# Kernel optimization log

Measured on AMD Instinct MI355X. Metric: run time of the kernel, lower is better.

## Reference

```python
import math
import jax, jax.numpy as jnp
import numpy as np

N_ORDERS = 2
CHUNK = 64  # tokens per chunk (before virtual-token expansion)


def _expand_derivative(x, n):
    """expand_virtual_tokens(mode='derivative'): [B,H,S,D] -> [B,H,S*n,D]."""
    B, H, S, D = x.shape
    pad = jnp.zeros((B, H, n - 1, D), x.dtype)
    xp = jnp.concatenate([pad, x], axis=2)  # [B,H,S+n-1,D]
    coeffs = np.array([(-1) ** kk * math.comb(n - 1, kk) for kk in range(n)], dtype=np.float32)
    coeffs = coeffs / np.abs(coeffs).sum()  # L1-normalized binomial coeffs
    # window j at token t is x_pad[t+j]*coeffs[j]; then flip window dim (as in torch .flip(-1))
    win = jnp.stack([xp[:, :, j:j + S, :] * coeffs[j] for j in range(n)], axis=3)  # [B,H,S,n,D]
    win = win[:, :, :, ::-1, :]
    return win.reshape(B, H, S * n, D)


def _unlinear(x, scale=2.0):
    """unlinear_activation: gated norm-scaled gelu applied to inter-chunk state."""
    xn = jnp.linalg.norm(x, axis=-1, keepdims=True) + 1e-6
    return x / scale * jax.nn.gelu(scale * x / xn, approximate=True)


def _stab(x):
    # ensure_stability: clamp to [-1e4, 1e4], nan -> center (0)
    return jnp.nan_to_num(jnp.clip(x, -1e4, 1e4), nan=0.0, posinf=1e4, neginf=-1e4)


def _forward(q, k, v, beta):
    n = N_ORDERS
    B, H, S, D = q.shape
    qe = _expand_derivative(q, n)
    ke = _expand_derivative(k, n)
    ve = _expand_derivative(v, n)
    be = jnp.repeat(beta, n, axis=-1)[..., None]  # [B,H,S*n,1]
    w = ke * be  # delta-rule write keys
    u = ve * be  # delta-rule write values

    Cn = CHUNK * n                     # virtual tokens per chunk
    NC = (S * n) // Cn                 # number of chunks
    ch = lambda x: x.reshape(B, H, NC, Cn, D)
    qc, kc, wc, uc = ch(qe), ch(ke), ch(w), ch(u)

    # triangular (forward-substitution) inversion per chunk:
    # T = (I + tril(W K^T, -1))^{-1}  == fast_invert_matrix of the strictly-lower system
    A = jnp.tril(jnp.einsum('bhnid,bhnjd->bhnij', wc, kc), -1)
    eye = jnp.eye(Cn, dtype=q.dtype)
    T = jax.scipy.linalg.solve_triangular(
        eye + A, jnp.broadcast_to(eye, A.shape), lower=True, unit_diagonal=True)
    wci = jnp.einsum('bhnij,bhnjd->bhnid', T, wc)
    uci = jnp.einsum('bhnij,bhnjd->bhnid', T, uc)

    def chunk_step(h, xs):
        # sequential_delta_product_scan body: per-token Householder updates, n_orders steps
        qx, wx, ux = xs  # each [B,H,Cn,D]
        C = CHUNK
        qr = qx.reshape(B, H, C, n, D)
        wr = wx.reshape(B, H, C, n, D)
        ur = ux.reshape(B, H, C, n, D)
        state = jnp.broadcast_to(h[:, :, None], (B, H, C, D, D))  # per-token state
        outs = []
        for s in range(n):
            qs, ws, us = qr[:, :, :, s], wr[:, :, :, s], ur[:, :, :, s]
            kho = jnp.einsum('bhcd,bhcde->bhce', ws, state)
            uval = us - kho
            o_inter = jnp.einsum('bhcd,bhcde->bhce', qs, state)
            o_intra = qs * uval
            state = _stab(state + jnp.einsum('bhcd,bhce->bhcde', ws, uval))
            outs.append(o_intra + o_inter)
        o = jnp.stack(outs, axis=3).reshape(B, H, C * n, D)  # interleave: pos t*n+s
        h_new = _unlinear(state[:, :, -1])  # linear_activation=False path
        return h_new, o

    xs = (jnp.moveaxis(qc, 2, 0), jnp.moveaxis(wci, 2, 0), jnp.moveaxis(uci, 2, 0))
    h0 = jnp.zeros((B, H, D, D), q.dtype)
    _, os = jax.lax.scan(chunk_step, h0, xs)  # os: [NC,B,H,Cn,D]
    out_v = jnp.moveaxis(os, 0, 2).reshape(B, H, S, n, D)
    return out_v[..., n - 1, :]  # collapse virtual tokens: keep last-order output per token


def setup_inputs() -> dict:
    key = jax.random.key(0)
    kq, kk, kv, kb = jax.random.split(key, 4)
    B, H, S, D = 2, 16, 2048, 64
    return {
        'q': jax.random.normal(kq, (B, H, S, D), jnp.float32),
        'k': jax.random.normal(kk, (B, H, S, D), jnp.float32),
        'v': jax.random.normal(kv, (B, H, S, D), jnp.float32),
        'beta': jax.random.uniform(kb, (B, H, S), jnp.float32),
    }


def reference(q, k, v, beta):
    return _forward(q, k, v, beta)
```

## Files before the change

kernel.cpp:

```cpp
#include <hip/hip_runtime.h>
#include <math.h>


namespace {
constexpr int PAIRS = 32;
constexpr int SLEN  = 2048;
constexpr int D     = 64;
constexpr int CK    = 64;
constexpr int CN    = 128;
constexpr int NCH   = 32;
constexpr int NB2   = 16;
constexpr int NP    = 5;
constexpr size_t YWORDS = (size_t)PAIRS * NCH * CN * CN;
constexpr int GP = 2145;

__device__ __forceinline__ float stab1(float x) {
    float y = __builtin_amdgcn_fmed3f(x, -10000.f, 10000.f);
    return (x != x) ? 0.f : y;
}

__device__ __forceinline__ int kidx(int a, int f4) {
    return a * 68 + 4 * (f4 ^ ((a >> 2) & 3));
}
}

__global__ __launch_bounds__(256, 2)
void la_gram(const float* __restrict__ kg, float* __restrict__ gG)
{
    __shared__ float kstf[65 * 68];
    const int blk = blockIdx.x;
    const int p = blk >> 5, nc = blk & 31;
    const int tid = threadIdx.x;
    const int baseT = nc * CK;
    const float* kp = kg + (size_t)p * SLEN * D;

    for (int u = tid; u < 65 * 16; u += 256) {
        int a = u >> 4, f4 = u & 15;
        int src = baseT - 1 + a;
        float4 val = float4{0.f, 0.f, 0.f, 0.f};
        if (src >= 0) val = ((const float4*)(kp + (size_t)src * D))[f4];
        *(float4*)&kstf[kidx(a, f4)] = val;
    }
    __syncthreads();

    float* gps = gG + (size_t)blk * GP;
    for (int tt = tid; tt < 17 * 17; tt += 256) {
        int ta = tt / 17, tb = tt % 17;
        if (tb > ta) continue;
        int a0 = ta * 4, b0 = tb * 4;
        float acc[4][4] = {};
        for (int d4 = 0; d4 < 16; ++d4) {
            float4 av[4], bv[4];
            #pragma unroll
            for (int r = 0; r < 4; ++r) {
                av[r] = *(const float4*)&kstf[kidx(min(a0 + r, 64), d4)];
                bv[r] = *(const float4*)&kstf[kidx(min(b0 + r, 64), d4)];
            }
            #pragma unroll
            for (int r = 0; r < 4; ++r)
                #pragma unroll
                for (int c = 0; c < 4; ++c)
                    acc[r][c] += av[r].x * bv[c].x + av[r].y * bv[c].y
                               + av[r].z * bv[c].z + av[r].w * bv[c].w;
        }
        #pragma unroll
        for (int r = 0; r < 4; ++r)
            #pragma unroll
            for (int c = 0; c < 4; ++c) {
                int a = a0 + r, b = b0 + c;
                if (a <= 64 && b <= a)
                    gps[a * (a + 1) / 2 + b] = acc[r][c];
            }
    }
}

__global__ __launch_bounds__(256, 3)
void la_phase1g(const float* __restrict__ kg, const float* __restrict__ vg,
                const float* __restrict__ bg, float* __restrict__ ws,
                const float* __restrict__ gG)
{
    __shared__ float Ysh[CN][64];
    __shared__ float scm[2][CN][8];
    __shared__ float redsh[24][66];
    __shared__ float bq4[CK], bh[CK];

    const int blk  = blockIdx.x;
    const int p    = blk >> 6;
    const int nc   = (blk >> 1) & 31;
    const int half = blk & 1;
    const int tid  = threadIdx.x;
    const int col  = tid & 63;
    const int m    = tid >> 6;
    const int baseT = nc * CK;
    const float* kp = kg + (size_t)p * SLEN * D;
    const float* vp = vg + (size_t)p * SLEN * D;
    const float* bp = bg + (size_t)p * SLEN;
    const float* gps = gG + (size_t)(p * NCH + nc) * GP;

    if (tid < CK) {
        float bv = bp[baseT + tid];
        bq4[tid] = 0.25f * bv;
        bh[tid]  = 0.5f  * bv;
    }
    __syncthreads();

    const float* srcBase = half ? vp : kp;
    for (int u = tid; u < CN * 16; u += 256) {
        int i = u >> 4, f4 = u & 15;
        int ci = i >> 1, si = i & 1;
        float sc = si ? bh[ci] : -bh[ci];
        int srcT = baseT + ci - si;
        float4 val = float4{0.f, 0.f, 0.f, 0.f};
        if (srcT >= 0) val = ((const float4*)(srcBase + (size_t)srcT * D))[f4];
        val.x *= sc; val.y *= sc; val.z *= sc; val.w *= sc;
        *(float4*)&Ysh[i][f4 * 4] = val;
    }
    for (int e = tid; e < 64; e += 256) {
        int j = e >> 3, r = e & 7;
        int ai = (r >> 1) - (r & 1) + 1;
        int aj = (j >> 1) - (j & 1) + 1;
        int amax = max(ai, aj), amin = min(ai, aj);
        float sgn = ((r ^ j) & 1) ? -1.f : 1.f;
        scm[0][j][r] = sgn * bq4[r >> 1] * gps[amax * (amax + 1) / 2 + amin];
    }
    __syncthreads();

    for (int g = 0; g < 16; ++g) {
        const int buf = g & 1;
        float acc[8] = {};
        for (int j = m; j < 8 * g; j += 4) {
            float yv = Ysh[j][col];
            const float4 a03 = *(const float4*)&scm[buf][j][0];
            const float4 a47 = *(const float4*)&scm[buf][j][4];
            acc[0] += a03.x * yv; acc[1] += a03.y * yv;
            acc[2] += a03.z * yv; acc[3] += a03.w * yv;
            acc[4] += a47.x * yv; acc[5] += a47.y * yv;
            acc[6] += a47.z * yv; acc[7] += a47.w * yv;
        }
        if (m > 0) {
            #pragma unroll
            for (int r = 0; r < 8; ++r) redsh[(m - 1) * 8 + r][col] = acc[r];
        }
        __syncthreads();
        if (m == 0) {
            if (g > 0) {
                #pragma unroll
                for (int r = 0; r < 8; ++r)
                    acc[r] += redsh[r][col] + redsh[8 + r][col] + redsh[16 + r][col];
            }
            float yn[8];
            #pragma unroll
            for (int r = 0; r < 8; ++r) {
                float val = Ysh[8 * g + r][col] - acc[r];
                #pragma unroll
                for (int rp = 0; rp < 8; ++rp)
                    if (rp < r) val -= scm[buf][8 * g + rp][r] * yn[rp];
                yn[r] = val;
                Ysh[8 * g + r][col] = val;
            }
        } else if (g < 15) {
            const int T = g + 1, bufB = T & 1;
            const int nel = 8 * (8 * T + 8);
            for (int e = tid - 64; e < nel; e += 192) {
                int j = e >> 3, r = e & 7;
                int i = 8 * T + r;
                int ai = (i >> 1) - (i & 1) + 1;
                int aj = (j >> 1) - (j & 1) + 1;
                int amax = max(ai, aj), amin = min(ai, aj);
                float sgn = ((i ^ j) & 1) ? -1.f : 1.f;
                scm[bufB][j][r] = sgn * bq4[i >> 1] * gps[amax * (amax + 1) / 2 + amin];
            }
        }
        __syncthreads();
    }

    float* gY = ws + (size_t)(p * NCH + nc) * (CN * CN) + half * 64;
    for (int u = tid; u < CN * 16; u += 256) {
        int r = u >> 4, f4 = u & 15;
        *(float4*)&gY[r * CN + f4 * 4] = *(const float4*)&Ysh[r][f4 * 4];
    }
}

__global__ __launch_bounds__(256, 2)
void la_phase1f(const float* __restrict__ kg, const float* __restrict__ vg,
                const float* __restrict__ bg, float* __restrict__ ws)
{
    __shared__ float Ysh[CN][64];
    __shared__ float Gm[65][66];
    __shared__ char  ureg[17680];
    __shared__ float bq4[CK], bh[CK];

    float* kstf = (float*)ureg;
    float* scm  = (float*)ureg;
    float (*redsh)[66] = (float(*)[66])(ureg + 8192);

    const int blk  = blockIdx.x;
    const int p    = blk >> 6;
    const int nc   = (blk >> 1) & 31;
    const int half = blk & 1;
    const int tid  = threadIdx.x;
    const int baseT = nc * CK;
    const float* kp = kg + (size_t)p * SLEN * D;
    const float* vp = vg + (size_t)p * SLEN * D;
    const float* bp = bg + (size_t)p * SLEN;

    for (int u = tid; u < 65 * 16; u += 256) {
        int a = u >> 4, f4 = u & 15;
        int src = baseT - 1 + a;
        float4 val = float4{0.f, 0.f, 0.f, 0.f};
        if (src >= 0) val = ((const float4*)(kp + (size_t)src * D))[f4];
        *(float4*)&kstf[kidx(a, f4)] = val;
    }
    if (tid < CK) {
        float bv = bp[baseT + tid];
        bq4[tid] = 0.25f * bv;
        bh[tid]  = 0.5f  * bv;
    }
    __syncthreads();

    for (int u = tid; u < CN * 16; u += 256) {
        int i = u >> 4, f4 = u & 15;
        int ci = i >> 1, si = i & 1;
        float sc = si ? bh[ci] : -bh[ci];
        float4 val = float4{0.f, 0.f, 0.f, 0.f};
        if (half == 0) {
            val = *(const float4*)&kstf[kidx(ci - si + 1, f4)];
        } else {
            int srcT = baseT + ci - si;
            if (srcT >= 0) val = ((const float4*)(vp + (size_t)srcT * D))[f4];
        }
        val.x *= sc; val.y *= sc; val.z *= sc; val.w *= sc;
        *(float4*)&Ysh[i][f4 * 4] = val;
    }

    for (int tt = tid; tt < 17 * 17; tt += 256) {
        int ta = tt / 17, tb = tt % 17;
        if (tb > ta) continue;
        int a0 = ta * 4, b0 = tb * 4;
        float acc[4][4] = {};
        for (int d4 = 0; d4 < 16; ++d4) {
            float4 av[4], bv[4];
            #pragma unroll
            for (int r = 0; r < 4; ++r) {
                av[r] = *(const float4*)&kstf[kidx(min(a0 + r, 64), d4)];
                bv[r] = *(const float4*)&kstf[kidx(min(b0 + r, 64), d4)];
            }
            #pragma unroll
            for (int r = 0; r < 4; ++r)
                #pragma unroll
                for (int c = 0; c < 4; ++c)
                    acc[r][c] += av[r].x * bv[c].x + av[r].y * bv[c].y
                               + av[r].z * bv[c].z + av[r].w * bv[c].w;
        }
        #pragma unroll
        for (int r = 0; r < 4; ++r)
            #pragma unroll
            for (int c = 0; c < 4; ++c)
                if (a0 + r <= 64 && b0 + c <= 64) {
                    Gm[a0 + r][b0 + c] = acc[r][c];
                    Gm[b0 + c][a0 + r] = acc[r][c];
                }
    }
    __syncthreads();

    auto stripf = [&](int g, int t0, int tstride) {
        int buf = g & 1;
        int jmax = 8 * g + 8;
        for (int e = t0; e < 8 * jmax; e += tstride) {
            int j = e >> 3, r = e & 7;
            int i = 8 * g + r;
            int ai = (i >> 1) - (i & 1) + 1;
            int aj = (j >> 1) - (j & 1) + 1;
            float sgn = ((i ^ j) & 1) ? -1.f : 1.f;
            scm[(buf * CN + j) * 8 + r] = sgn * bq4[i >> 1] * Gm[ai][aj];
        }
    };

    stripf(0, tid, 256);
    __syncthreads();

    const int col = tid & 63;
    const int m   = tid >> 6;
    for (int g = 0; g < 16; ++g) {
        const int buf = g & 1;
        float acc[8] = {};
        for (int j = m; j < 8 * g; j += 4) {
            float yv = Ysh[j][col];
            const float4 a03 = *(const float4*)&scm[(buf * CN + j) * 8];
            const float4 a47 = *(const float4*)&scm[(buf * CN + j) * 8 + 4];
            acc[0] += a03.x * yv; acc[1] += a03.y * yv;
            acc[2] += a03.z * yv; acc[3] += a03.w * yv;
            acc[4] += a47.x * yv; acc[5] += a47.y * yv;
            acc[6] += a47.z * yv; acc[7] += a47.w * yv;
        }
        if (m > 0) {
            #pragma unroll
            for (int r = 0; r < 8; ++r) redsh[(m - 1) * 8 + r][col] = acc[r];
        }
        __syncthreads();
        if (m == 0) {
            if (g > 0) {
                #pragma unroll
                for (int r = 0; r < 8; ++r)
                    acc[r] += redsh[r][col] + redsh[8 + r][col] + redsh[16 + r][col];
            }
            float yn[8];
            #pragma unroll
            for (int r = 0; r < 8; ++r) {
                float val = Ysh[8 * g + r][col] - acc[r];
                #pragma unroll
                for (int rp = 0; rp < 8; ++rp)
                    if (rp < r) val -= scm[(buf * CN + 8 * g + rp) * 8 + r] * yn[rp];
                yn[r] = val;
                Ysh[8 * g + r][col] = val;
            }
        } else if (g < 15) {
            stripf(g + 1, tid - 64, 192);
        }
        __syncthreads();
    }

    float* gY = ws + (size_t)(p * NCH + nc) * (CN * CN) + half * 64;
    for (int u = tid; u < CN * 16; u += 256) {
        int r = u >> 4, f4 = u & 15;
        *(float4*)&gY[r * CN + f4 * 4] = *(const float4*)&Ysh[r][f4 * 4];
    }
}

__global__ __launch_bounds__(512, 4)
void la_phase2(const float* __restrict__ qg, const float* __restrict__ ws,
               float* __restrict__ outg)
{
    __shared__ float WU[2][NP][256];
    __shared__ float Qs[2][NP][64];
    __shared__ float pR1[8][NP][64];
    __shared__ float pKH[8][NP][64];
    __shared__ float pOA[8][NP][64];
    __shared__ float UV0[NP][64];
    __shared__ float UV1r[64];
    __shared__ float hsh[64][67];

    const int blk  = blockIdx.x;
    const int p    = blk >> 4, nb = blk & 15;
    const int tid  = threadIdx.x;
    const int w    = tid >> 6, lane = tid & 63;
    const int hd   = tid >> 3;
    const int he0  = (tid & 7) * 8;

    const float* qp = qg + (size_t)p * SLEN * D;
    float* op = outg + (size_t)p * SLEN * D;
    const float* wsbase = ws + (size_t)p * NCH * (CN * CN);

    const int cMain = nb * 4 + w;

    float4 wuR = float4{0.f, 0.f, 0.f, 0.f};
    float  qR  = 0.f;

    auto stage_load = [&](int nc) {
        const float* gY = wsbase + (size_t)nc * (CN * CN);
        if (w < 4) {
            wuR = *(const float4*)(gY + (size_t)(2 * cMain) * CN + lane * 4);
            int t = nc * CK + cMain;
            qR = qp[(size_t)((t > 0) ? t - 1 : 0) * D + lane];
        } else if (w == 4) {
            wuR = *(const float4*)(gY + (size_t)126 * CN + lane * 4);
            qR = qp[(size_t)(nc * CK + 62) * D + lane];
        }
    };
    auto stage_write = [&](int buf) {
        if (w < NP) {
            *(float4*)&WU[buf][w][lane * 4] = wuR;
            Qs[buf][w][lane] = qR;
        }
    };

    for (int idx = tid; idx < 64 * 67; idx += 512) (&hsh[0][0])[idx] = 0.f;
    stage_load(0);
    stage_write(0);
    __syncthreads();

    for (int nc = 0; nc < NCH; ++nc) {
        const int buf = nc & 1;

        float hs[8];
        #pragma unroll
        for (int j = 0; j < 8; ++j) hs[j] = hsh[8 * w + j][lane];

        if (nc + 1 < NCH) stage_load(nc + 1);

        #pragma unroll
        for (int P = 0; P < NP; ++P) {
            float4 a = *(const float4*)&WU[buf][P][8 * w];
            float4 b = *(const float4*)&WU[buf][P][8 * w + 4];
            pR1[w][P][lane] =
                  ((a.x * hs[0] + a.y * hs[1]) + (a.z * hs[2] + a.w * hs[3]))
                + ((b.x * hs[4] + b.y * hs[5]) + (b.z * hs[6] + b.w * hs[7]));
        }
        __syncthreads();

        if (w < NP) {
            float s = 0.f;
            #pragma unroll
            for (int wv = 0; wv < 8; ++wv) s += pR1[wv][w][lane];
            UV0[w][lane] = WU[buf][w][64 + lane] - s;
        }
        __syncthreads();

        #pragma unroll
        for (int P = 0; P < NP; ++P) {
            float uv0 = UV0[P][lane];
            float4 w0a = *(const float4*)&WU[buf][P][8 * w];
            float4 w0b = *(const float4*)&WU[buf][P][8 * w + 4];
            float4 w1a = *(const float4*)&WU[buf][P][128 + 8 * w];
            float4 w1b = *(const float4*)&WU[buf][P][128 + 8 * w + 4];
            float4 qa  = *(const float4*)&Qs[buf][P][8 * w];
            float4 qb  = *(const float4*)&Qs[buf][P][8 * w + 4];
            float st0 = stab1(hs[0] + w0a.x * uv0);
            float st1 = stab1(hs[1] + w0a.y * uv0);
            float st2 = stab1(hs[2] + w0a.z * uv0);
            float st3 = stab1(hs[3] + w0a.w * uv0);
            float st4 = stab1(hs[4] + w0b.x * uv0);
            float st5 = stab1(hs[5] + w0b.y * uv0);
            float st6 = stab1(hs[6] + w0b.z * uv0);
            float st7 = stab1(hs[7] + w0b.w * uv0);
            pKH[w][P][lane] =
                  ((w1a.x * st0 + w1a.y * st1) + (w1a.z * st2 + w1a.w * st3))
                + ((w1b.x * st4 + w1b.y * st5) + (w1b.z * st6 + w1b.w * st7));
            pOA[w][P][lane] =
                  ((qa.x * st0 + qa.y * st1) + (qa.z * st2 + qa.w * st3))
                + ((qb.x * st4 + qb.y * st5) + (qb.z * st6 + qb.w * st7));
        }
        stage_write(buf ^ 1);
        __syncthreads();

        if (w < 4) {
            float skh = 0.f, soa = 0.f;
            #pragma unroll
            for (int wv = 0; wv < 8; ++wv) {
                skh += pKH[wv][w][lane];
                soa += pOA[wv][w][lane];
            }
            float uv1 = WU[buf][w][192 + lane] - skh;
            int t = nc * CK + cMain;
            float outv = 0.5f * (Qs[buf][w][lane] * uv1 + soa);
            op[(size_t)t * D + lane] = (t > 0) ? outv : 0.f;
        } else if (w == 4) {
            float skh = 0.f;
            #pragma unroll
            for (int wv = 0; wv < 8; ++wv) skh += pKH[wv][4][lane];
            UV1r[lane] = WU[buf][4][192 + lane] - skh;
        }
        __syncthreads();

        {
            float w0d = WU[buf][4][hd];
            float w1d = WU[buf][4][128 + hd];
            float st2v[8];
            float ssum = 0.f;
            #pragma unroll
            for (int j = 0; j < 8; ++j) {
                float st1 = stab1(hsh[hd][he0 + j] + w0d * UV0[4][he0 + j]);
                float st2 = stab1(st1 + w1d * UV1r[he0 + j]);
                st2v[j] = st2;
                ssum += st2 * st2;
            }
            ssum += __shfl_xor(ssum, 1);
            ssum += __shfl_xor(ssum, 2);
            ssum += __shfl_xor(ssum, 4);
            float xn = __builtin_amdgcn_sqrtf(ssum) + 1e-6f;
            float s2 = 2.f * __builtin_amdgcn_rcpf(xn);
            #pragma unroll
            for (int j = 0; j < 8; ++j) {
                float x  = st2v[j];
                float y  = x * s2;
                float y2 = y * y;
                float e  = __builtin_amdgcn_exp2f(y * (2.3022078f + 0.1029432f * y2));
                float th = (e - 1.f) * __builtin_amdgcn_rcpf(e + 1.f);
                hsh[hd][he0 + j] = 0.25f * x * y * (1.f + th);
            }
        }
        __syncthreads();
    }
}

extern "C" void kernel_launch(void* const* d_in, const int* in_sizes, int n_in,
                              void* d_out, int out_size, void* d_ws, size_t ws_size,
                              hipStream_t stream)
{
    (void)in_sizes; (void)n_in; (void)out_size;
    const float* q    = (const float*)d_in[0];
    const float* k    = (const float*)d_in[1];
    const float* v    = (const float*)d_in[2];
    const float* beta = (const float*)d_in[3];
    float* ws  = (float*)d_ws;
    float* out = (float*)d_out;

    const size_t need = (YWORDS + (size_t)PAIRS * NCH * GP) * sizeof(float);
    if (ws_size >= need) {
        float* gG = ws + YWORDS;
        la_gram<<<PAIRS * NCH, 256, 0, stream>>>(k, gG);
        la_phase1g<<<PAIRS * NCH * 2, 256, 0, stream>>>(k, v, beta, ws, gG);
    } else {
        la_phase1f<<<PAIRS * NCH * 2, 256, 0, stream>>>(k, v, beta, ws);
    }
    la_phase2<<<PAIRS * NB2, 512, 0, stream>>>(q, ws, out);
}
```

Measured before the change: 260.9 us.

## Split sequential phase into lean state scan plus chunk-parallel output kernel

Replaces the fused phase2 kernel with two kernels. la_scan walks the chunks in order, using only the last two virtual tokens per chunk to carry the inter-chunk state, and writes every chunk's starting state to workspace. la_out then computes per-token outputs in parallel over all pairs×chunks. This shortens the serial critical path and exposes more parallelism, at the cost of an extra launch and a round trip of the state through global memory. The workspace for the states reuses the gram buffer region once it is no longer needed.

```diff
diff --git a/kernel.cpp b/kernel.cpp
--- a/kernel.cpp
+++ b/kernel.cpp
@@ -13,6 +13,8 @@
 constexpr int NP    = 5;
 constexpr size_t YWORDS = (size_t)PAIRS * NCH * CN * CN;
 constexpr int GP = 2145;
+constexpr size_t GGW = (size_t)PAIRS * NCH * GP;
+constexpr size_t HGW = (size_t)PAIRS * (NCH + 1) * D * D;
 
 __device__ __forceinline__ float stab1(float x) {
     float y = __builtin_amdgcn_fmed3f(x, -10000.f, 10000.f);
@@ -178,6 +180,178 @@
     for (int u = tid; u < CN * 16; u += 256) {
         int r = u >> 4, f4 = u & 15;
         *(float4*)&gY[r * CN + f4 * 4] = *(const float4*)&Ysh[r][f4 * 4];
+    }
+}
+
+__global__ __launch_bounds__(512, 1)
+void la_scan(const float* __restrict__ ws, float* __restrict__ hg)
+{
+    __shared__ float w0s[64], u0s[64], w1s[64], u1s[64];
+    __shared__ float pA[8][64], pB[8][64];
+    __shared__ float hsh2[64][67];
+
+    const int p = blockIdx.x;
+    const int tid = threadIdx.x;
+    const int w = tid >> 6, lane = tid & 63;
+    const int hd = tid >> 3, he0 = (tid & 7) * 8;
+    const float* Yp = ws + (size_t)p * NCH * (CN * CN);
+    float* hp = hg + (size_t)p * (NCH + 1) * (D * D);
+
+    for (int idx = tid; idx < D * D; idx += 512) hp[idx] = 0.f;
+    for (int idx = tid; idx < 64 * 67; idx += 512) (&hsh2[0][0])[idx] = 0.f;
+
+    auto stagew = [&](float v) {
+        if (tid < 64)       w0s[tid] = v;
+        else if (tid < 128) u0s[tid - 64] = v;
+        else if (tid < 192) w1s[tid - 128] = v;
+        else if (tid < 256) u1s[tid - 192] = v;
+    };
+    {
+        float v = 0.f;
+        if (tid < 256) v = Yp[(size_t)(126 + (tid >> 7)) * CN + (tid & 127)];
+        stagew(v);
+    }
+    float hs[8];
+    #pragma unroll
+    for (int j = 0; j < 8; ++j) hs[j] = 0.f;
+    __syncthreads();
+
+    for (int nc = 0; nc < NCH; ++nc) {
+        float pf = 0.f;
+        if (nc + 1 < NCH && tid < 256)
+            pf = Yp[(size_t)(nc + 1) * (CN * CN)
+                    + (size_t)(126 + (tid >> 7)) * CN + (tid & 127)];
+
+        float s = 0.f;
+        #pragma unroll
+        for (int j = 0; j < 8; ++j) s += w0s[8 * w + j] * hs[j];
+        pA[w][lane] = s;
+        __syncthreads();
+
+        float sum = 0.f;
+        #pragma unroll
+        for (int wv = 0; wv < 8; ++wv) sum += pA[wv][lane];
+        const float uv0 = u0s[lane] - sum;
+
+        float st1[8];
+        float s2 = 0.f;
+        #pragma unroll
+        for (int j = 0; j < 8; ++j) {
+            st1[j] = stab1(hs[j] + w0s[8 * w + j] * uv0);
+            s2 += w1s[8 * w + j] * st1[j];
+        }
+        pB[w][lane] = s2;
+        __syncthreads();
+
+        float sum2 = 0.f;
+        #pragma unroll
+        for (int wv = 0; wv < 8; ++wv) sum2 += pB[wv][lane];
+        const float uv1 = u1s[lane] - sum2;
+        #pragma unroll
+        for (int j = 0; j < 8; ++j)
+            hsh2[8 * w + j][lane] = stab1(st1[j] + w1s[8 * w + j] * uv1);
+        __syncthreads();
+
+        {
+            float st2v[8];
+            float ssum = 0.f;
+            #pragma unroll
+            for (int j = 0; j < 8; ++j) {
+                st2v[j] = hsh2[hd][he0 + j];
+                ssum += st2v[j] * st2v[j];
+            }
+            ssum += __shfl_xor(ssum, 1);
+            ssum += __shfl_xor(ssum, 2);
+            ssum += __shfl_xor(ssum, 4);
+            float xn = __builtin_amdgcn_sqrtf(ssum) + 1e-6f;
+            float sc2 = 2.f * __builtin_amdgcn_rcpf(xn);
+            float hn[8];
+            #pragma unroll
+            for (int j = 0; j < 8; ++j) {
+                float x  = st2v[j];
+                float y  = x * sc2;
+                float y2 = y * y;
+                float e  = __builtin_amdgcn_exp2f(y * (2.3022078f + 0.1029432f * y2));
+                float th = (e - 1.f) * __builtin_amdgcn_rcpf(e + 1.f);
+                hn[j] = 0.25f * x * y * (1.f + th);
+                hsh2[hd][he0 + j] = hn[j];
+            }
+            float* ho = hp + (size_t)(nc + 1) * (D * D) + hd * 64 + he0;
+            *(float4*)&ho[0] = float4{hn[0], hn[1], hn[2], hn[3]};
+            *(float4*)&ho[4] = float4{hn[4], hn[5], hn[6], hn[7]};
+        }
+        if (nc + 1 < NCH) stagew(pf);
+        __syncthreads();
+        #pragma unroll
+        for (int j = 0; j < 8; ++j) hs[j] = hsh2[8 * w + j][lane];
+    }
+}
+
+__global__ __launch_bounds__(512)
+void la_out(const float* __restrict__ qg, const float* __restrict__ ws,
+            const float* __restrict__ hg, float* __restrict__ outg)
+{
+    __shared__ float hT[64 * 68];
+    __shared__ float wbr[8][3][64];
+
+    const int blk = blockIdx.x;
+    const int p = blk >> 5, nc = blk & 31;
+    const int tid = threadIdx.x;
+    const int w = tid >> 6, lane = tid & 63;
+
+    const float* Yc = ws + (size_t)(p * NCH + nc) * (CN * CN);
+    const float* hp = hg + ((size_t)p * (NCH + 1) + nc) * (D * D);
+    const float* qp = qg + (size_t)p * SLEN * D;
+    float* op = outg + (size_t)p * SLEN * D;
+
+    for (int idx = tid; idx < D * D; idx += 512) {
+        int d = idx >> 6, e = idx & 63;
+        hT[e * 68 + d] = hp[idx];
+    }
+    __syncthreads();
+
+    float4 hr[16];
+    #pragma unroll
+    for (int k = 0; k < 16; ++k)
+        hr[k] = *(const float4*)&hT[lane * 68 + 4 * k];
+
+    for (int it = 0; it < 8; ++it) {
+        const int c = it * 8 + w;
+        const int t = nc * CK + c;
+        const int srcT = (t > 0) ? t - 1 : 0;
+
+        const float w0v = Yc[(size_t)(2 * c) * CN + lane];
+        const float u0l = Yc[(size_t)(2 * c) * CN + 64 + lane];
+        const float w1v = Yc[(size_t)(2 * c + 1) * CN + lane];
+        const float u1l = Yc[(size_t)(2 * c + 1) * CN + 64 + lane];
+        const float qv  = qp[(size_t)srcT * D + lane];
+        wbr[w][0][lane] = w0v;
+        wbr[w][1][lane] = w1v;
+        wbr[w][2][lane] = qv;
+
+        float uv0 = u0l;
+        #pragma unroll
+        for (int k = 0; k < 16; ++k) {
+            float4 wb = *(const float4*)&wbr[w][0][4 * k];
+            uv0 -= (wb.x * hr[k].x + wb.y * hr[k].y)
+                 + (wb.z * hr[k].z + wb.w * hr[k].w);
+        }
+        float kh = 0.f, oa = 0.f;
+        #pragma unroll
+        for (int k = 0; k < 16; ++k) {
+            float4 wb0 = *(const float4*)&wbr[w][0][4 * k];
+            float4 wb1 = *(const float4*)&wbr[w][1][4 * k];
+            float4 qb  = *(const float4*)&wbr[w][2][4 * k];
+            float st0 = stab1(hr[k].x + wb0.x * uv0);
+            float st1 = stab1(hr[k].y + wb0.y * uv0);
+            float st2 = stab1(hr[k].z + wb0.z * uv0);
+            float st3 = stab1(hr[k].w + wb0.w * uv0);
+            kh += (wb1.x * st0 + wb1.y * st1) + (wb1.z * st2 + wb1.w * st3);
+            oa += (qb.x * st0 + qb.y * st1) + (qb.z * st2 + qb.w * st3);
+        }
+        float uv1 = u1l - kh;
+        float outv = 0.5f * (qv * uv1 + oa);
+        op[(size_t)t * D + lane] = (t > 0) ? outv : 0.f;
     }
 }
 
@@ -381,11 +555,9 @@
 
     for (int nc = 0; nc < NCH; ++nc) {
         const int buf = nc & 1;
-
         float hs[8];
         #pragma unroll
         for (int j = 0; j < 8; ++j) hs[j] = hsh[8 * w + j][lane];
-
         if (nc + 1 < NCH) stage_load(nc + 1);
 
         #pragma unroll
@@ -495,13 +667,24 @@
     float* ws  = (float*)d_ws;
     float* out = (float*)d_out;
 
-    const size_t need = (YWORDS + (size_t)PAIRS * NCH * GP) * sizeof(float);
-    if (ws_size >= need) {
+    const size_t maxW  = (HGW > GGW) ? HGW : GGW;
+    const size_t needA = (YWORDS + maxW) * sizeof(float);
+    const size_t needB = (YWORDS + GGW) * sizeof(float);
+
+    if (ws_size >= needA) {
+        float* gG = ws + YWORDS;
+        float* hg = ws + YWORDS;
+        la_gram<<<PAIRS * NCH, 256, 0, stream>>>(k, gG);
+        la_phase1g<<<PAIRS * NCH * 2, 256, 0, stream>>>(k, v, beta, ws, gG);
+        la_scan<<<PAIRS, 512, 0, stream>>>(ws, hg);
+        la_out<<<PAIRS * NCH, 512, 0, stream>>>(q, ws, hg, out);
+    } else if (ws_size >= needB) {
         float* gG = ws + YWORDS;
         la_gram<<<PAIRS * NCH, 256, 0, stream>>>(k, gG);
         la_phase1g<<<PAIRS * NCH * 2, 256, 0, stream>>>(k, v, beta, ws, gG);
+        la_phase2<<<PAIRS * NB2, 512, 0, stream>>>(q, ws, out);
     } else {
         la_phase1f<<<PAIRS * NCH * 2, 256, 0, stream>>>(k, v, beta, ws);
-    }
-    la_phase2<<<PAIRS * NB2, 512, 0, stream>>>(q, ws, out);
-}
+        la_phase2<<<PAIRS * NB2, 512, 0, stream>>>(q, ws, out);
+    }
+}
```

Result: slower. 270.8 us (+3.8%).
